# Kernel optimization log

Hardware: AMD Instinct MI355X
Metric: run time of the kernel (lower is better)

Reference implementation:

```python
import jax, jax.numpy as jnp
import numpy as np

K = 512
D = 256


def setup_inputs() -> dict:
    key = jax.random.key(0)
    k1, k2 = jax.random.split(key)
    z_e = jax.random.normal(k1, (64, D, 32, 32), dtype=jnp.float32)
    # torch init: uniform_(-1/K, 1/K)
    codebook = jax.random.uniform(k2, (K, D), dtype=jnp.float32, minval=-1.0 / K, maxval=1.0 / K)
    return {"z_e": z_e, "codebook": codebook}


def reference(z_e, codebook):
    B, C, H, W = z_e.shape
    # (B,C,H,W) -> (B,H,W,C) -> (N,D)
    z_flat = jnp.transpose(z_e, (0, 2, 3, 1)).reshape(-1, C)
    # squared L2 distances: ||z||^2 + ||e||^2 - 2 z.e  -> [N, K]
    d = (jnp.sum(z_flat ** 2, axis=1, keepdims=True)
         + jnp.sum(codebook ** 2, axis=1)
         - 2.0 * jnp.matmul(z_flat, codebook.T))
    idx = jnp.argmin(d, axis=1)  # [N]
    z_q_flat = codebook[idx]  # [N, D] gather
    z_q = jnp.transpose(z_q_flat.reshape(B, H, W, C), (0, 3, 1, 2))
    commitment_loss = jnp.mean((z_e - jax.lax.stop_gradient(z_q)) ** 2)
    codebook_loss = jnp.mean((z_q - jax.lax.stop_gradient(z_e)) ** 2)
    # straight-through estimator
    z_q_st = z_e + jax.lax.stop_gradient(z_q - z_e)
    indices = idx.reshape(B, H, W)
    return (z_q_st, commitment_loss, codebook_loss, indices)
```

## Files before the change

### kernel.cpp

```cpp
#include <hip/hip_runtime.h>


typedef __attribute__((ext_vector_type(8))) short short8v;
typedef __attribute__((ext_vector_type(4))) float float4v;
typedef unsigned short ushort_t;

namespace {
constexpr int K = 512;
constexpr int D = 256;
constexpr int HW = 1024;
constexpr int NROWS = 65536;
constexpr int CHW = D * HW;

constexpr int ZQ_SIZE = 64 * CHW;
constexpr int LOSS0_OFF = ZQ_SIZE;
constexpr int LOSS1_OFF = ZQ_SIZE + 1;
constexpr int IDX_OFF = ZQ_SIZE + 2;

constexpr int WS_EH_FLOATS = (K * D) / 2;
constexpr int WS_B = WS_EH_FLOATS;
constexpr int WS_PART = WS_B + K;
constexpr int NBLK = NROWS / 32;

constexpr float EPS_CAND = 3.0e-3f;
constexpr int MAXC = 16;
}

__device__ __forceinline__ ushort_t bf16_rne(float f) {
    unsigned u = __float_as_uint(f);
    u += 0x7fffu + ((u >> 16) & 1u);
    return (ushort_t)(u >> 16);
}

__global__ void vq_prep(const float* __restrict__ cb, float* __restrict__ ws) {
    const int k = blockIdx.x;
    const int t = threadIdx.x;
    ushort_t* eh = (ushort_t*)ws;
    eh[(size_t)k * D + t] = bf16_rne(cb[k * D + t]);
    __shared__ float r16[16];
    if (t < 16) {
#pragma clang fp contract(off)
        const float* x = cb + k * D + (t >> 3) * 128;
        const int j = t & 7;
        float v = x[j];
        float r = v * v;
        for (int i = 1; i < 16; ++i) {
            float w = x[8 * i + j];
            r += w * w;
        }
        r16[t] = r;
    }
    __syncthreads();
    if (t == 0) {
#pragma clang fp contract(off)
        float lo = ((r16[0] + r16[1]) + (r16[2] + r16[3])) +
                   ((r16[4] + r16[5]) + (r16[6] + r16[7]));
        float hi = ((r16[8] + r16[9]) + (r16[10] + r16[11])) +
                   ((r16[12] + r16[13]) + (r16[14] + r16[15]));
        ws[WS_B + k] = lo + hi;
    }
}

__global__ __launch_bounds__(256, 5) void vq_mega(
    const float* __restrict__ z_e, const float* __restrict__ cb,
    const ushort_t* __restrict__ eh, const float* __restrict__ Bv,
    float* __restrict__ part, float* __restrict__ out) {
    __shared__ __align__(16) ushort_t zh[32][264];
    __shared__ float lds_B[K];
    __shared__ float scr[32][17];
    __shared__ int cand[32][MAXC];
    __shared__ float lds_A[32];
    __shared__ float wmin[4][32];
    __shared__ float rmin[32];
    __shared__ int cnt[32];
    __shared__ float wpart[4];

    const int t = threadIdx.x;
    const int row0 = blockIdx.x * 32;
    const int b = row0 >> 10;
    const int hw0 = row0 & 1023;
    const float* zbase = z_e + (size_t)b * CHW + hw0;

    lds_B[t] = Bv[t];
    lds_B[t + 256] = Bv[t + 256];

    {
#pragma clang fp contract(off)
        const int row = t & 31;
        const int q = t >> 5;
        const int half = q >> 2;
        const int j0 = (q & 3) * 2;
        const float* zp = zbase + row + (size_t)(half * 128) * HW;
        float v0 = zp[(size_t)j0 * HW];
        float v1 = zp[(size_t)(j0 + 1) * HW];
        float r0 = v0 * v0;
        float r1 = v1 * v1;
        for (int i = 1; i < 16; ++i) {
            float w0 = zp[(size_t)(8 * i + j0) * HW];
            float w1 = zp[(size_t)(8 * i + j0 + 1) * HW];
            r0 += w0 * w0;
            r1 += w1 * w1;
        }
        scr[row][half * 8 + j0] = r0;
        scr[row][half * 8 + j0 + 1] = r1;
    }

    {
        const int row = t & 31;
        const int dc = t >> 5;
        const float* zp = zbase + row;
#pragma unroll
        for (int i = 0; i < 8; ++i) {
            const int d4 = dc * 32 + i * 4;
            float f0 = zp[(size_t)(d4 + 0) * HW];
            float f1 = zp[(size_t)(d4 + 1) * HW];
            float f2 = zp[(size_t)(d4 + 2) * HW];
            float f3 = zp[(size_t)(d4 + 3) * HW];
            uint2 ph;
            ph.x = (unsigned)bf16_rne(f0) | ((unsigned)bf16_rne(f1) << 16);
            ph.y = (unsigned)bf16_rne(f2) | ((unsigned)bf16_rne(f3) << 16);
            *reinterpret_cast<uint2*>(&zh[row][d4]) = ph;
        }
    }
    __syncthreads();
    if (t < 32) {
#pragma clang fp contract(off)
        const float* r = scr[t];
        float lo = ((r[0] + r[1]) + (r[2] + r[3])) + ((r[4] + r[5]) + (r[6] + r[7]));
        float hi = ((r[8] + r[9]) + (r[10] + r[11])) + ((r[12] + r[13]) + (r[14] + r[15]));
        lds_A[t] = lo + hi;
    }
    __syncthreads();

    const int lane = t & 63;
    const int w = t >> 6;
    const int wc0 = w * 128;
    const int l15 = lane & 15;
    const int kg = lane >> 4;

    float4v acc[8][2];
#pragma unroll
    for (int c = 0; c < 8; ++c)
#pragma unroll
        for (int rt = 0; rt < 2; ++rt) acc[c][rt] = (float4v)0.f;

    const ushort_t* ehp = eh + (size_t)(wc0 + l15) * D + 8 * kg;

#pragma unroll 4
    for (int d0 = 0; d0 < D; d0 += 32) {
        const short8v bh0 = *reinterpret_cast<const short8v*>(&zh[l15][d0 + 8 * kg]);
        const short8v bh1 = *reinterpret_cast<const short8v*>(&zh[16 + l15][d0 + 8 * kg]);
#pragma unroll
        for (int c = 0; c < 8; ++c) {
            const short8v a = *reinterpret_cast<const short8v*>(ehp + c * 16 * D + d0);
            acc[c][0] = __builtin_amdgcn_mfma_f32_16x16x32_bf16(a, bh0, acc[c][0], 0, 0, 0);
            acc[c][1] = __builtin_amdgcn_mfma_f32_16x16x32_bf16(a, bh1, acc[c][1], 0, 0, 0);
        }
    }

    float lmin0 = 3.0e38f, lmin1 = 3.0e38f;
#pragma unroll
    for (int c = 0; c < 8; ++c)
#pragma unroll
        for (int rt = 0; rt < 2; ++rt)
#pragma unroll
            for (int r = 0; r < 4; ++r) {
                const int code = wc0 + 16 * c + 4 * kg + r;
                const int row = rt * 16 + l15;
                float s = (lds_A[row] + lds_B[code]) - 2.0f * acc[c][rt][r];
                acc[c][rt][r] = s;
                if (rt == 0) lmin0 = fminf(lmin0, s);
                else lmin1 = fminf(lmin1, s);
            }
    lmin0 = fminf(lmin0, __shfl_xor(lmin0, 16));
    lmin0 = fminf(lmin0, __shfl_xor(lmin0, 32));
    lmin1 = fminf(lmin1, __shfl_xor(lmin1, 16));
    lmin1 = fminf(lmin1, __shfl_xor(lmin1, 32));
    if (lane < 16) {
        wmin[w][l15] = lmin0;
        wmin[w][16 + l15] = lmin1;
    }
    __syncthreads();
    if (t < 32) {
        rmin[t] = fminf(fminf(wmin[0][t], wmin[1][t]), fminf(wmin[2][t], wmin[3][t]));
        cnt[t] = 0;
    }
    __syncthreads();

#pragma unroll
    for (int c = 0; c < 8; ++c)
#pragma unroll
        for (int rt = 0; rt < 2; ++rt) {
            const int row = rt * 16 + l15;
            const float thr = rmin[row] + EPS_CAND;
#pragma unroll
            for (int r = 0; r < 4; ++r) {
                if (acc[c][rt][r] <= thr) {
                    const int code = wc0 + 16 * c + 4 * kg + r;
                    int slot = atomicAdd(&cnt[row], 1);
                    if (slot < MAXC) cand[row][slot] = code;
                }
            }
        }
    __syncthreads();

    float* ed = reinterpret_cast<float*>(&zh[0][0]);
    int* ek = reinterpret_cast<int*>(ed + 256);
    int* kb = ek + 256;
    {
        const int row = t & 31;
        const int ct = t >> 5;
        const float* zp = zbase + row;
        const int n = cnt[row];
        float bd = 3.0e38f;
        int bk = 0x7fffffff;
        if (n == 1) {
            if (ct == 0) {
                bd = -3.0e38f;
                bk = cand[row][0];
            }
        } else {
            const bool full = (n > MAXC);
            const int lim = full ? K : n;
            for (int s = ct; s < lim; s += 8) {
                const int k = full ? s : cand[row][s];
                const float* ep = cb + (size_t)k * D;
                float a = 0.f;
#pragma unroll 8
                for (int c = 0; c < D; ++c) a = fmaf(zp[(size_t)c * HW], ep[c], a);
                float dv;
                {
#pragma clang fp contract(off)
                    float t1 = lds_A[row] + lds_B[k];
                    dv = t1 - 2.0f * a;
                }
                if (dv < bd || (dv == bd && k < bk)) {
                    bd = dv;
                    bk = k;
                }
            }
        }
        ed[t] = bd;
        ek[t] = bk;
    }
    __syncthreads();
    if (t < 32) {
        float bd = ed[t];
        int bk = ek[t];
#pragma unroll
        for (int q = 1; q < 8; ++q) {
            float od = ed[q * 32 + t];
            int ok = ek[q * 32 + t];
            if (od < bd || (od == bd && ok < bk)) {
                bd = od;
                bk = ok;
            }
        }
        kb[t] = bk;
        out[IDX_OFF + row0 + t] = (float)bk;
    }
    __syncthreads();

    {
        const int j = t & 31;
        const int g = t >> 5;
        const int kme = kb[j];
        const float* ep = cb + (size_t)kme * D;
        const float* zp = zbase + j;
        float* ob = out + (size_t)b * CHW + hw0 + j;
        float accum = 0.f;
#pragma unroll 4
        for (int i = 0; i < 32; ++i) {
            const int c = g * 32 + i;
            float z = zp[(size_t)c * HW];
            float e = ep[c];
            ob[(size_t)c * HW] = z + (e - z);
            float df = z - e;
            accum = fmaf(df, df, accum);
        }
#pragma unroll
        for (int m = 1; m < 64; m <<= 1) accum += __shfl_xor(accum, m);
        if ((t & 63) == 0) wpart[t >> 6] = accum;
    }
    __syncthreads();
    if (t == 0) part[blockIdx.x] = (wpart[0] + wpart[1]) + (wpart[2] + wpart[3]);
}

__global__ void vq_finish(const float* __restrict__ part, float* __restrict__ out) {
    const int t = threadIdx.x;
    double s = 0.0;
#pragma unroll
    for (int i = 0; i < 8; ++i) s += (double)part[t + 256 * i];
#pragma unroll
    for (int m = 1; m < 64; m <<= 1) s += __shfl_xor(s, m);
    __shared__ double wsum[4];
    if ((t & 63) == 0) wsum[t >> 6] = s;
    __syncthreads();
    if (t == 0) {
        double mean = (wsum[0] + wsum[1] + wsum[2] + wsum[3]) / (double)ZQ_SIZE;
        out[LOSS0_OFF] = (float)mean;
        out[LOSS1_OFF] = (float)mean;
    }
}

extern "C" void kernel_launch(void* const* d_in, const int* in_sizes, int n_in,
                              void* d_out, int out_size, void* d_ws, size_t ws_size,
                              hipStream_t stream) {
    const float* z_e = (const float*)d_in[0];
    const float* cb = (const float*)d_in[1];
    float* out = (float*)d_out;
    float* ws = (float*)d_ws;

    const ushort_t* eh = (const ushort_t*)ws;
    float* Bv = ws + WS_B;
    float* part = ws + WS_PART;

    vq_prep<<<K, D, 0, stream>>>(cb, ws);
    vq_mega<<<NBLK, 256, 0, stream>>>(z_e, cb, eh, Bv, part, out);
    vq_finish<<<1, 256, 0, stream>>>(part, out);
}
```

Measured before the change: 139.9 us.

## Split argmin and gather into separate kernels with vectorized gather pass

```diff
diff --git a/kernel.cpp b/kernel.cpp
--- a/kernel.cpp
+++ b/kernel.cpp
@@ -19,8 +19,11 @@
 
 constexpr int WS_EH_FLOATS = (K * D) / 2;
 constexpr int WS_B = WS_EH_FLOATS;
-constexpr int WS_PART = WS_B + K;
-constexpr int NBLK = NROWS / 32;
+constexpr int WS_KIDX = WS_B + K;
+constexpr int WS_PART = WS_KIDX + NROWS;
+
+constexpr int NBLK_A = NROWS / 32;
+constexpr int NBLK_G = 2048;
 
 constexpr float EPS_CAND = 3.0e-3f;
 constexpr int MAXC = 16;
@@ -61,10 +64,10 @@
     }
 }
 
-__global__ __launch_bounds__(256, 5) void vq_mega(
+__global__ __launch_bounds__(256, 6) void vq_argmin2(
     const float* __restrict__ z_e, const float* __restrict__ cb,
     const ushort_t* __restrict__ eh, const float* __restrict__ Bv,
-    float* __restrict__ part, float* __restrict__ out) {
+    int* __restrict__ wsidx, float* __restrict__ out) {
     __shared__ __align__(16) ushort_t zh[32][264];
     __shared__ float lds_B[K];
     __shared__ float scr[32][17];
@@ -73,7 +76,6 @@
     __shared__ float wmin[4][32];
     __shared__ float rmin[32];
     __shared__ int cnt[32];
-    __shared__ float wpart[4];
 
     const int t = threadIdx.x;
     const int row0 = blockIdx.x * 32;
@@ -85,42 +87,34 @@
     lds_B[t + 256] = Bv[t + 256];
 
     {
-#pragma clang fp contract(off)
         const int row = t & 31;
         const int q = t >> 5;
         const int half = q >> 2;
         const int j0 = (q & 3) * 2;
-        const float* zp = zbase + row + (size_t)(half * 128) * HW;
-        float v0 = zp[(size_t)j0 * HW];
-        float v1 = zp[(size_t)(j0 + 1) * HW];
-        float r0 = v0 * v0;
-        float r1 = v1 * v1;
-        for (int i = 1; i < 16; ++i) {
-            float w0 = zp[(size_t)(8 * i + j0) * HW];
-            float w1 = zp[(size_t)(8 * i + j0 + 1) * HW];
-            r0 += w0 * w0;
-            r1 += w1 * w1;
+        const int cbase = half * 128;
+        const float* zp = zbase + row;
+        float r0, r1;
+        {
+#pragma clang fp contract(off)
+            const int c0 = cbase + j0;
+            float w0 = zp[(size_t)c0 * HW];
+            float w1 = zp[(size_t)(c0 + 1) * HW];
+            r0 = w0 * w0;
+            r1 = w1 * w1;
+            *reinterpret_cast<unsigned*>(&zh[row][c0]) =
+                (unsigned)bf16_rne(w0) | ((unsigned)bf16_rne(w1) << 16);
+            for (int i = 1; i < 16; ++i) {
+                const int c = cbase + 8 * i + j0;
+                float u0 = zp[(size_t)c * HW];
+                float u1 = zp[(size_t)(c + 1) * HW];
+                r0 += u0 * u0;
+                r1 += u1 * u1;
+                *reinterpret_cast<unsigned*>(&zh[row][c]) =
+                    (unsigned)bf16_rne(u0) | ((unsigned)bf16_rne(u1) << 16);
+            }
         }
         scr[row][half * 8 + j0] = r0;
         scr[row][half * 8 + j0 + 1] = r1;
-    }
-
-    {
-        const int row = t & 31;
-        const int dc = t >> 5;
-        const float* zp = zbase + row;
-#pragma unroll
-        for (int i = 0; i < 8; ++i) {
-            const int d4 = dc * 32 + i * 4;
-            float f0 = zp[(size_t)(d4 + 0) * HW];
-            float f1 = zp[(size_t)(d4 + 1) * HW];
-            float f2 = zp[(size_t)(d4 + 2) * HW];
-            float f3 = zp[(size_t)(d4 + 3) * HW];
-            uint2 ph;
-            ph.x = (unsigned)bf16_rne(f0) | ((unsigned)bf16_rne(f1) << 16);
-            ph.y = (unsigned)bf16_rne(f2) | ((unsigned)bf16_rne(f3) << 16);
-            *reinterpret_cast<uint2*>(&zh[row][d4]) = ph;
-        }
     }
     __syncthreads();
     if (t < 32) {
@@ -130,7 +124,6 @@
         float hi = ((r[8] + r[9]) + (r[10] + r[11])) + ((r[12] + r[13]) + (r[14] + r[15]));
         lds_A[t] = lo + hi;
     }
-    __syncthreads();
 
     const int lane = t & 63;
     const int w = t >> 6;
@@ -157,6 +150,7 @@
             acc[c][1] = __builtin_amdgcn_mfma_f32_16x16x32_bf16(a, bh1, acc[c][1], 0, 0, 0);
         }
     }
+    __syncthreads();
 
     float lmin0 = 3.0e38f, lmin1 = 3.0e38f;
 #pragma unroll
@@ -206,7 +200,6 @@
 
     float* ed = reinterpret_cast<float*>(&zh[0][0]);
     int* ek = reinterpret_cast<int*>(ed + 256);
-    int* kb = ek + 256;
     {
         const int row = t & 31;
         const int ct = t >> 5;
@@ -256,34 +249,55 @@
                 bk = ok;
             }
         }
-        kb[t] = bk;
+        wsidx[row0 + t] = bk;
         out[IDX_OFF + row0 + t] = (float)bk;
     }
-    __syncthreads();
-
-    {
-        const int j = t & 31;
-        const int g = t >> 5;
-        const int kme = kb[j];
-        const float* ep = cb + (size_t)kme * D;
-        const float* zp = zbase + j;
-        float* ob = out + (size_t)b * CHW + hw0 + j;
-        float accum = 0.f;
-#pragma unroll 4
-        for (int i = 0; i < 32; ++i) {
-            const int c = g * 32 + i;
-            float z = zp[(size_t)c * HW];
-            float e = ep[c];
-            ob[(size_t)c * HW] = z + (e - z);
-            float df = z - e;
-            accum = fmaf(df, df, accum);
-        }
-#pragma unroll
-        for (int m = 1; m < 64; m <<= 1) accum += __shfl_xor(accum, m);
-        if ((t & 63) == 0) wpart[t >> 6] = accum;
-    }
-    __syncthreads();
-    if (t == 0) part[blockIdx.x] = (wpart[0] + wpart[1]) + (wpart[2] + wpart[3]);
+}
+
+__global__ __launch_bounds__(256, 8) void vq_gather2(
+    const float* __restrict__ z_e, const float* __restrict__ cb,
+    const int* __restrict__ wsidx, float* __restrict__ part,
+    float* __restrict__ out) {
+    __shared__ float wpart[4];
+    const int t = threadIdx.x;
+    const int blk = blockIdx.x;
+    const int cg = blk & 7;
+    const int q = (blk >> 3) & 3;
+    const int b = blk >> 5;
+    const int lane = t & 63;
+    const int csub = t >> 6;
+    const int hw = q * 256 + lane * 4;
+
+    const int4 kk = *reinterpret_cast<const int4*>(&wsidx[b * HW + hw]);
+    const float* e0 = cb + (size_t)kk.x * D;
+    const float* e1 = cb + (size_t)kk.y * D;
+    const float* e2 = cb + (size_t)kk.z * D;
+    const float* e3 = cb + (size_t)kk.w * D;
+    const size_t zoff = (size_t)b * CHW + hw;
+
+    float accum = 0.f;
+#pragma unroll 2
+    for (int i = 0; i < 8; ++i) {
+        const int c = cg * 32 + csub * 8 + i;
+        const size_t off = zoff + (size_t)c * HW;
+        const float4 z4 = *reinterpret_cast<const float4*>(&z_e[off]);
+        const float ex = e0[c], ey = e1[c], ez = e2[c], ew = e3[c];
+        float4 o4;
+        o4.x = z4.x + (ex - z4.x);
+        o4.y = z4.y + (ey - z4.y);
+        o4.z = z4.z + (ez - z4.z);
+        o4.w = z4.w + (ew - z4.w);
+        *reinterpret_cast<float4*>(&out[off]) = o4;
+        accum = fmaf(z4.x - ex, z4.x - ex, accum);
+        accum = fmaf(z4.y - ey, z4.y - ey, accum);
+        accum = fmaf(z4.z - ez, z4.z - ez, accum);
+        accum = fmaf(z4.w - ew, z4.w - ew, accum);
+    }
+#pragma unroll
+    for (int m = 1; m < 64; m <<= 1) accum += __shfl_xor(accum, m);
+    if (lane == 0) wpart[csub] = accum;
+    __syncthreads();
+    if (t == 0) part[blk] = (wpart[0] + wpart[1]) + (wpart[2] + wpart[3]);
 }
 
 __global__ void vq_finish(const float* __restrict__ part, float* __restrict__ out) {
@@ -313,9 +327,11 @@
 
     const ushort_t* eh = (const ushort_t*)ws;
     float* Bv = ws + WS_B;
+    int* wsidx = (int*)(ws + WS_KIDX);
     float* part = ws + WS_PART;
 
     vq_prep<<<K, D, 0, stream>>>(cb, ws);
-    vq_mega<<<NBLK, 256, 0, stream>>>(z_e, cb, eh, Bv, part, out);
+    vq_argmin2<<<NBLK_A, 256, 0, stream>>>(z_e, cb, eh, Bv, wsidx, out);
+    vq_gather2<<<NBLK_G, 256, 0, stream>>>(z_e, cb, wsidx, part, out);
     vq_finish<<<1, 256, 0, stream>>>(part, out);
 }
```

After: 215.0 us. 53.8% more time.
